# Optimization experiments

Measured on AMD Instinct MI355X. Metric: run time of the kernel, lower is better.

Reference implementation:

```python
import jax, jax.numpy as jnp
import numpy as np

EMBED_DIM = 768
NUM_HEADS = 12
HEAD_DIM = EMBED_DIM // NUM_HEADS
BSZ = 8
N = 1024


def setup_inputs() -> dict:
    key = jax.random.key(0)
    ks = jax.random.split(key, 11)
    s = 1.0 / np.sqrt(EMBED_DIM)
    return {
        "query": jax.random.normal(ks[0], (BSZ, N, EMBED_DIM), dtype=jnp.float32),
        "attn_bias": jax.random.normal(ks[1], (BSZ, NUM_HEADS, N, N), dtype=jnp.float32),
        "Wq": jax.random.normal(ks[2], (EMBED_DIM, EMBED_DIM), dtype=jnp.float32) * s,
        "bq": jax.random.normal(ks[3], (EMBED_DIM,), dtype=jnp.float32) * 0.01,
        "Wk": jax.random.normal(ks[4], (EMBED_DIM, EMBED_DIM), dtype=jnp.float32) * s,
        "bk": jax.random.normal(ks[5], (EMBED_DIM,), dtype=jnp.float32) * 0.01,
        "Wv": jax.random.normal(ks[6], (EMBED_DIM, EMBED_DIM), dtype=jnp.float32) * s,
        "bv": jax.random.normal(ks[7], (EMBED_DIM,), dtype=jnp.float32) * 0.01,
        "Wo": jax.random.normal(ks[8], (EMBED_DIM, EMBED_DIM), dtype=jnp.float32) * s,
        "bo": jnp.zeros((EMBED_DIM,), dtype=jnp.float32),
    }


def reference(query, attn_bias, Wq, bq, Wk, bk, Wv, bv, Wo, bo):
    # query: (b, n, e); weights stored torch-style (out, in): y = x @ W.T + b
    b, n, e = query.shape
    h, d = NUM_HEADS, HEAD_DIM
    scaling = d ** -0.5

    q = (query @ Wq.T + bq) * scaling          # (b, n, e)
    k = query @ Wk.T + bk
    v = query @ Wv.T + bv

    # split heads -> (b, h, n, d)
    q = q.reshape(b, n, h, d).transpose(0, 2, 1, 3)
    k = k.reshape(b, n, h, d).transpose(0, 2, 1, 3)
    v = v.reshape(b, n, h, d).transpose(0, 2, 1, 3)

    scores = jnp.einsum("bhqd,bhkd->bhqk", q, k) + attn_bias  # (b, h, n, n)
    probs = jax.nn.softmax(scores, axis=-1)
    attn = jnp.einsum("bhqk,bhkd->bhqd", probs, v)             # (b, h, n, d)

    attn = attn.transpose(0, 2, 1, 3).reshape(b, n, e)
    return attn @ Wo.T + bo
```

## Files before the change

kernel.cpp:

```cpp
#include <hip/hip_runtime.h>
#include <math.h>


namespace {

constexpr int kB = 8, kN = 1024, kE = 768, kH = 12, kD = 64;
constexpr int kM = kB * kN;
constexpr int kNX = kM * kE;
constexpr int kNW = kE * kE;
constexpr int kTot = kNX + 4 * kNW;

typedef short bf16x8 __attribute__((ext_vector_type(8)));
typedef float f32x4 __attribute__((ext_vector_type(4)));

__device__ __forceinline__ ushort f2bf(float x) {
  uint u = __float_as_uint(x);
  u += 0x7fffu + ((u >> 16) & 1u);
  return (ushort)(u >> 16);
}
__device__ __forceinline__ float bf2f(ushort h) {
  return __uint_as_float(((uint)h) << 16);
}

__global__ __launch_bounds__(256)
void split_convert(const float* __restrict__ X, const float* __restrict__ Wq,
                   const float* __restrict__ Wk, const float* __restrict__ Wv,
                   const float* __restrict__ Wo, ushort* __restrict__ Xh,
                   ushort* __restrict__ Xl, ushort* __restrict__ Wh,
                   ushort* __restrict__ Wl) {
  const int gid = blockIdx.x * 256 + threadIdx.x;
  const int i4 = gid * 4;
  if (i4 >= kTot) return;
  const float* s;
  ushort *dh, *dl;
  if (i4 < kNX) {
    s = X + i4;
    dh = Xh + i4;
    dl = Xl + i4;
  } else {
    const int j = i4 - kNX;
    const int w = j / kNW;
    const int o = j - w * kNW;
    s = (w == 0) ? Wq + o : (w == 1) ? Wk + o : (w == 2) ? Wv + o : Wo + o;
    dh = Wh + j;
    dl = Wl + j;
  }
  const float4 v = *(const float4*)s;
  ushort4 h, l;
  h.x = f2bf(v.x);
  h.y = f2bf(v.y);
  h.z = f2bf(v.z);
  h.w = f2bf(v.w);
  l.x = f2bf(v.x - bf2f(h.x));
  l.y = f2bf(v.y - bf2f(h.y));
  l.z = f2bf(v.z - bf2f(h.z));
  l.w = f2bf(v.w - bf2f(h.w));
  *(ushort4*)dh = h;
  *(ushort4*)dl = l;
}

__global__ __launch_bounds__(256)
void split_attn(const float* __restrict__ A, ushort* __restrict__ Ah,
                ushort* __restrict__ Al) {
  const int i4 = (blockIdx.x * 256 + threadIdx.x) * 4;
  if (i4 >= kNX) return;
  const float4 v = *(const float4*)(A + i4);
  ushort4 h, l;
  h.x = f2bf(v.x);
  h.y = f2bf(v.y);
  h.z = f2bf(v.z);
  h.w = f2bf(v.w);
  l.x = f2bf(v.x - bf2f(h.x));
  l.y = f2bf(v.y - bf2f(h.y));
  l.z = f2bf(v.z - bf2f(h.z));
  l.w = f2bf(v.w - bf2f(h.w));
  *(ushort4*)(Ah + i4) = h;
  *(ushort4*)(Al + i4) = l;
}

struct Frag44 {
  f32x4 a[4][4];
};

template <typename EPI>
__device__ __forceinline__ void gemm_core(const ushort* __restrict__ Ahg,
                                          const ushort* __restrict__ Alg,
                                          const ushort* __restrict__ Bhg,
                                          const ushort* __restrict__ Blg,
                                          int m0, int o0, EPI epi) {
  __shared__ ushort Ah[128][40], Al[128][40], Bh[128][40], Bl[128][40];
  const int tid = threadIdx.x;
  const int wid = tid >> 6, lane = tid & 63;
  const int wm = wid >> 1, wn = wid & 1;
  const int g = lane >> 4, lr = lane & 15;

  f32x4 acc[4][4];
#pragma unroll
  for (int i = 0; i < 4; ++i)
#pragma unroll
    for (int j = 0; j < 4; ++j) acc[i][j] = (f32x4)0.f;

  for (int k0 = 0; k0 < kE; k0 += 32) {
#pragma unroll
    for (int p = 0; p < 4; ++p) {
      const int f = tid + p * 256;
      const int m = f >> 3, kq = f & 7;
      const int ga = (m0 + m) * kE + k0 + kq * 4;
      const int gb = (o0 + m) * kE + k0 + kq * 4;
      *(uint2*)&Ah[m][kq * 4] = *(const uint2*)&Ahg[ga];
      *(uint2*)&Al[m][kq * 4] = *(const uint2*)&Alg[ga];
      *(uint2*)&Bh[m][kq * 4] = *(const uint2*)&Bhg[gb];
      *(uint2*)&Bl[m][kq * 4] = *(const uint2*)&Blg[gb];
    }
    __syncthreads();

    bf16x8 ah[4], al[4];
#pragma unroll
    for (int mi = 0; mi < 4; ++mi) {
      const int ar = wm * 64 + mi * 16 + lr;
      ah[mi] = *reinterpret_cast<const bf16x8*>(&Ah[ar][g * 8]);
      al[mi] = *reinterpret_cast<const bf16x8*>(&Al[ar][g * 8]);
    }
#pragma unroll
    for (int nj = 0; nj < 4; ++nj) {
      const int br = wn * 64 + nj * 16 + lr;
      const bf16x8 bh = *reinterpret_cast<const bf16x8*>(&Bh[br][g * 8]);
      const bf16x8 bl = *reinterpret_cast<const bf16x8*>(&Bl[br][g * 8]);
#pragma unroll
      for (int mi = 0; mi < 4; ++mi) {
        acc[mi][nj] = __builtin_amdgcn_mfma_f32_16x16x32_bf16(ah[mi], bh,
                                                              acc[mi][nj], 0, 0, 0);
        acc[mi][nj] = __builtin_amdgcn_mfma_f32_16x16x32_bf16(ah[mi], bl,
                                                              acc[mi][nj], 0, 0, 0);
        acc[mi][nj] = __builtin_amdgcn_mfma_f32_16x16x32_bf16(al[mi], bh,
                                                              acc[mi][nj], 0, 0, 0);
      }
    }
    __syncthreads();
  }

#pragma unroll
  for (int nj = 0; nj < 4; ++nj) {
    const int o = o0 + wn * 64 + nj * 16 + lr;
#pragma unroll
    for (int mi = 0; mi < 4; ++mi) {
      const int mbase = m0 + wm * 64 + mi * 16 + g * 4;
#pragma unroll
      for (int r = 0; r < 4; ++r) epi(mbase + r, o, acc[mi][nj][r]);
    }
  }
}

__global__ __launch_bounds__(256)
void qkv_gemm(const ushort* __restrict__ Xh, const ushort* __restrict__ Xl,
              const ushort* __restrict__ Wh, const ushort* __restrict__ Wl,
              const float* __restrict__ bq, const float* __restrict__ bk,
              const float* __restrict__ bv, float* __restrict__ Qo,
              float* __restrict__ Ko, float* __restrict__ Vo) {
  const int z = blockIdx.z;
  const ushort* WhZ = Wh + (size_t)z * kNW;
  const ushort* WlZ = Wl + (size_t)z * kNW;
  const float* bb = (z == 0) ? bq : (z == 1) ? bk : bv;
  float* Y = (z == 0) ? Qo : (z == 1) ? Ko : Vo;
  const float scale = (z == 0) ? 0.125f : 1.0f;

  gemm_core(Xh, Xl, WhZ, WlZ, blockIdx.x * 128, blockIdx.y * 128,
            [=](int m, int o, float v) {
              const int bi = m >> 10, n = m & 1023;
              const int h = o >> 6, d = o & 63;
              Y[(((size_t)bi * kH + h) * kN + n) * kD + d] = (v + bb[o]) * scale;
            });
}

__global__ __launch_bounds__(256)
void out_gemm(const ushort* __restrict__ Ahg, const ushort* __restrict__ Alg,
              const ushort* __restrict__ Wh, const ushort* __restrict__ Wl,
              const float* __restrict__ bo, float* __restrict__ Y) {
  gemm_core(Ahg, Alg, Wh, Wl, blockIdx.x * 128, blockIdx.y * 128,
            [=](int m, int o, float v) { Y[(size_t)m * kE + o] = v + bo[o]; });
}

__global__ __launch_bounds__(256)
void attn_kernel(const float* __restrict__ Q, const float* __restrict__ K,
                 const float* __restrict__ V, const float* __restrict__ bias,
                 float* __restrict__ Ao) {
  __shared__ float Qs[64][64];
  __shared__ float Ks[64][64];
  __shared__ float Vs[64][64];
  __shared__ float St[64][65];
  __shared__ float red[4][64];
  __shared__ float mrow[64], lrow[64], srow[64];

  const int n0 = blockIdx.x * 64;
  const int h = blockIdx.y, b = blockIdx.z;
  const int tid = threadIdx.x;
  const int ty = tid >> 4, tx = tid & 15;
  const int i0 = ty * 4, j0 = tx * 4, d0 = tx * 4;
  const int irow = tid & 63, qtr = tid >> 6;

  const size_t headoff = ((size_t)(b * kH + h)) * kN * kD;
  const float* __restrict__ Qh = Q + headoff;
  const float* __restrict__ Kh = K + headoff;
  const float* __restrict__ Vh = V + headoff;
  const float* __restrict__ biash = bias + ((size_t)(b * kH + h)) * kN * kN;

#pragma unroll
  for (int p = 0; p < 4; ++p) {
    const int r = (tid >> 4) + p * 16;
    const int dq = (tid & 15) * 4;
    const float4 v4 = *(const float4*)&Qh[(size_t)(n0 + r) * kD + dq];
    Qs[dq + 0][r] = v4.x;
    Qs[dq + 1][r] = v4.y;
    Qs[dq + 2][r] = v4.z;
    Qs[dq + 3][r] = v4.w;
  }
  if (tid < 64) {
    mrow[tid] = -__builtin_inff();
    lrow[tid] = 0.f;
  }
  float O[4][4];
#pragma unroll
  for (int i = 0; i < 4; ++i)
#pragma unroll
    for (int j = 0; j < 4; ++j) O[i][j] = 0.f;
  __syncthreads();

  for (int t = 0; t < 16; ++t) {
    const int jg = t * 64;
#pragma unroll
    for (int p = 0; p < 4; ++p) {
      const int r = (tid >> 4) + p * 16;
      const int dq = (tid & 15) * 4;
      const float4 kv = *(const float4*)&Kh[(size_t)(jg + r) * kD + dq];
      Ks[dq + 0][r] = kv.x;
      Ks[dq + 1][r] = kv.y;
      Ks[dq + 2][r] = kv.z;
      Ks[dq + 3][r] = kv.w;
      *(float4*)&Vs[r][dq] = *(const float4*)&Vh[(size_t)(jg + r) * kD + dq];
    }
    __syncthreads();

    float s[4][4];
#pragma unroll
    for (int i = 0; i < 4; ++i)
#pragma unroll
      for (int j = 0; j < 4; ++j) s[i][j] = 0.f;
    for (int d = 0; d < 64; ++d) {
      float a[4], kb[4];
      *(float4*)&a[0] = *(const float4*)&Qs[d][i0];
      *(float4*)&kb[0] = *(const float4*)&Ks[d][j0];
#pragma unroll
      for (int i = 0; i < 4; ++i)
#pragma unroll
        for (int j = 0; j < 4; ++j) s[i][j] = fmaf(a[i], kb[j], s[i][j]);
    }
#pragma unroll
    for (int i = 0; i < 4; ++i) {
      const float4 bv4 =
          *(const float4*)&biash[(size_t)(n0 + i0 + i) * kN + jg + j0];
      St[j0 + 0][i0 + i] = s[i][0] + bv4.x;
      St[j0 + 1][i0 + i] = s[i][1] + bv4.y;
      St[j0 + 2][i0 + i] = s[i][2] + bv4.z;
      St[j0 + 3][i0 + i] = s[i][3] + bv4.w;
    }
    __syncthreads();

    float pm = -__builtin_inff();
#pragma unroll
    for (int j = 0; j < 16; ++j) pm = fmaxf(pm, St[qtr * 16 + j][irow]);
    red[qtr][irow] = pm;
    __syncthreads();
    if (tid < 64) {
      const float tm = fmaxf(fmaxf(red[0][tid], red[1][tid]),
                             fmaxf(red[2][tid], red[3][tid]));
      const float mo = mrow[tid];
      const float mn = fmaxf(mo, tm);
      mrow[tid] = mn;
      srow[tid] = __expf(mo - mn);
    }
    __syncthreads();

    const float mi = mrow[irow];
    float ps = 0.f;
#pragma unroll
    for (int j = 0; j < 16; ++j) {
      const float e = __expf(St[qtr * 16 + j][irow] - mi);
      St[qtr * 16 + j][irow] = e;
      ps += e;
    }
    red[qtr][irow] = ps;
    __syncthreads();
    if (tid < 64)
      lrow[tid] = lrow[tid] * srow[tid] +
                  (red[0][tid] + red[1][tid] + red[2][tid] + red[3][tid]);

    float sf[4];
#pragma unroll
    for (int i = 0; i < 4; ++i) sf[i] = srow[i0 + i];
#pragma unroll
    for (int i = 0; i < 4; ++i)
#pragma unroll
      for (int j = 0; j < 4; ++j) O[i][j] *= sf[i];
#pragma unroll 8
    for (int j = 0; j < 64; ++j) {
      const float4 vv = *(const float4*)&Vs[j][d0];
      const float p0 = St[j][i0 + 0];
      const float p1 = St[j][i0 + 1];
      const float p2 = St[j][i0 + 2];
      const float p3 = St[j][i0 + 3];
      O[0][0] = fmaf(p0, vv.x, O[0][0]);
      O[0][1] = fmaf(p0, vv.y, O[0][1]);
      O[0][2] = fmaf(p0, vv.z, O[0][2]);
      O[0][3] = fmaf(p0, vv.w, O[0][3]);
      O[1][0] = fmaf(p1, vv.x, O[1][0]);
      O[1][1] = fmaf(p1, vv.y, O[1][1]);
      O[1][2] = fmaf(p1, vv.z, O[1][2]);
      O[1][3] = fmaf(p1, vv.w, O[1][3]);
      O[2][0] = fmaf(p2, vv.x, O[2][0]);
      O[2][1] = fmaf(p2, vv.y, O[2][1]);
      O[2][2] = fmaf(p2, vv.z, O[2][2]);
      O[2][3] = fmaf(p2, vv.w, O[2][3]);
      O[3][0] = fmaf(p3, vv.x, O[3][0]);
      O[3][1] = fmaf(p3, vv.y, O[3][1]);
      O[3][2] = fmaf(p3, vv.z, O[3][2]);
      O[3][3] = fmaf(p3, vv.w, O[3][3]);
    }
    __syncthreads();
  }

#pragma unroll
  for (int i = 0; i < 4; ++i) {
    const float inv = 1.0f / lrow[i0 + i];
    float4 r;
    r.x = O[i][0] * inv;
    r.y = O[i][1] * inv;
    r.z = O[i][2] * inv;
    r.w = O[i][3] * inv;
    *(float4*)&Ao[((size_t)b * kN + n0 + i0 + i) * kE + h * kD + d0] = r;
  }
}

}

extern "C" void kernel_launch(void* const* d_in, const int* in_sizes, int n_in,
                              void* d_out, int out_size, void* d_ws,
                              size_t ws_size, hipStream_t stream) {
  (void)in_sizes;
  (void)n_in;
  (void)out_size;
  (void)ws_size;
  const float* x = (const float*)d_in[0];
  const float* bias = (const float*)d_in[1];
  const float* Wq = (const float*)d_in[2];
  const float* bq = (const float*)d_in[3];
  const float* Wk = (const float*)d_in[4];
  const float* bk = (const float*)d_in[5];
  const float* Wv = (const float*)d_in[6];
  const float* bv = (const float*)d_in[7];
  const float* Wo = (const float*)d_in[8];
  const float* bo = (const float*)d_in[9];
  float* out = (float*)d_out;

  const size_t per = (size_t)kB * kH * kN * kD;
  float* q = (float*)d_ws;
  float* k = q + per;
  float* v = k + per;
  float* attn = v + per;
  ushort* Xh = (ushort*)(attn + per);
  ushort* Xl = Xh + kNX;
  ushort* Whs = Xl + kNX;
  ushort* Wls = Whs + 4 * (size_t)kNW;
  ushort* AttnH = Wls + 4 * (size_t)kNW;
  ushort* AttnL = AttnH + kNX;

  split_convert<<<kTot / 1024, 256, 0, stream>>>(x, Wq, Wk, Wv, Wo, Xh, Xl,
                                                 Whs, Wls);

  dim3 g1(kM / 128, kE / 128, 3);
  qkv_gemm<<<g1, 256, 0, stream>>>(Xh, Xl, Whs, Wls, bq, bk, bv, q, k, v);

  dim3 g2(kN / 64, kH, kB);
  attn_kernel<<<g2, 256, 0, stream>>>(q, k, v, bias, attn);

  split_attn<<<kNX / 1024, 256, 0, stream>>>(attn, AttnH, AttnL);

  dim3 g3(kM / 128, kE / 128);
  out_gemm<<<g3, 256, 0, stream>>>(AttnH, AttnL, Whs + 3 * (size_t)kNW,
                                   Wls + 3 * (size_t)kNW, bo, out);
}
```

Baseline: 1.086 ms.

## Rewrite attention with split-bf16 MFMA and fuse bf16 splitting into epilogues

Replaces the scalar FP32 attention kernel with a flash-style kernel that computes QK^T and PV using bf16 MFMA with hi/lo splitting (three products per step) to keep near-FP32 accuracy. The QKV GEMM epilogue now writes split bf16 Q, K and transposed V directly, and the attention kernel writes the split output, which removes the separate split_attn pass and the FP32 intermediate buffers. Blocks are mapped so that heads group by XCD. Softmax reductions use wave shuffles and per-wave LDS in place of block barriers, but K/V are read straight from global memory without LDS reuse and the epilogue stores are scalar and strided.

```diff
diff --git a/kernel.cpp b/kernel.cpp
--- a/kernel.cpp
+++ b/kernel.cpp
@@ -59,29 +59,6 @@
   *(ushort4*)dl = l;
 }
 
-__global__ __launch_bounds__(256)
-void split_attn(const float* __restrict__ A, ushort* __restrict__ Ah,
-                ushort* __restrict__ Al) {
-  const int i4 = (blockIdx.x * 256 + threadIdx.x) * 4;
-  if (i4 >= kNX) return;
-  const float4 v = *(const float4*)(A + i4);
-  ushort4 h, l;
-  h.x = f2bf(v.x);
-  h.y = f2bf(v.y);
-  h.z = f2bf(v.z);
-  h.w = f2bf(v.w);
-  l.x = f2bf(v.x - bf2f(h.x));
-  l.y = f2bf(v.y - bf2f(h.y));
-  l.z = f2bf(v.z - bf2f(h.z));
-  l.w = f2bf(v.w - bf2f(h.w));
-  *(ushort4*)(Ah + i4) = h;
-  *(ushort4*)(Al + i4) = l;
-}
-
-struct Frag44 {
-  f32x4 a[4][4];
-};
-
 template <typename EPI>
 __device__ __forceinline__ void gemm_core(const ushort* __restrict__ Ahg,
                                           const ushort* __restrict__ Alg,
@@ -155,21 +132,205 @@
 void qkv_gemm(const ushort* __restrict__ Xh, const ushort* __restrict__ Xl,
               const ushort* __restrict__ Wh, const ushort* __restrict__ Wl,
               const float* __restrict__ bq, const float* __restrict__ bk,
-              const float* __restrict__ bv, float* __restrict__ Qo,
-              float* __restrict__ Ko, float* __restrict__ Vo) {
+              const float* __restrict__ bv, ushort* __restrict__ Qh,
+              ushort* __restrict__ Ql, ushort* __restrict__ Kh,
+              ushort* __restrict__ Kl, ushort* __restrict__ Vth,
+              ushort* __restrict__ Vtl) {
   const int z = blockIdx.z;
   const ushort* WhZ = Wh + (size_t)z * kNW;
   const ushort* WlZ = Wl + (size_t)z * kNW;
   const float* bb = (z == 0) ? bq : (z == 1) ? bk : bv;
-  float* Y = (z == 0) ? Qo : (z == 1) ? Ko : Vo;
-  const float scale = (z == 0) ? 0.125f : 1.0f;
 
   gemm_core(Xh, Xl, WhZ, WlZ, blockIdx.x * 128, blockIdx.y * 128,
             [=](int m, int o, float v) {
               const int bi = m >> 10, n = m & 1023;
               const int h = o >> 6, d = o & 63;
-              Y[(((size_t)bi * kH + h) * kN + n) * kD + d] = (v + bb[o]) * scale;
+              const int head = bi * kH + h;
+              float val = v + bb[o];
+              if (z == 0) val *= 0.125f;
+              const ushort hi = f2bf(val);
+              const ushort lo = f2bf(val - bf2f(hi));
+              if (z == 2) {
+                const size_t idx = ((size_t)head * kD + d) * kN + n;
+                Vth[idx] = hi;
+                Vtl[idx] = lo;
+              } else {
+                const size_t idx = ((size_t)head * kN + n) * kD + d;
+                if (z == 0) {
+                  Qh[idx] = hi;
+                  Ql[idx] = lo;
+                } else {
+                  Kh[idx] = hi;
+                  Kl[idx] = lo;
+                }
+              }
             });
+}
+
+__global__ __launch_bounds__(256, 2)
+void attn_mfma(const ushort* __restrict__ Qhg, const ushort* __restrict__ Qlg,
+               const ushort* __restrict__ Khg, const ushort* __restrict__ Klg,
+               const ushort* __restrict__ Vth, const ushort* __restrict__ Vtl,
+               const float* __restrict__ bias, ushort* __restrict__ AoH,
+               ushort* __restrict__ AoL) {
+  __shared__ uint Plds[4][16 * 68];
+
+  const int lb = blockIdx.x;
+  const int xcd = lb & 7;
+  const int idx = lb >> 3;
+  const int lh = idx >> 4;
+  const int qb = idx & 15;
+  const int head = lh * 8 + xcd;
+  const int n0 = qb * 64;
+
+  const int tid = threadIdx.x;
+  const int w = tid >> 6, lane = tid & 63;
+  const int g = lane >> 4, c = lane & 15;
+
+  const size_t qkoff = (size_t)head * kN * kD;
+  const float* __restrict__ biash = bias + (size_t)head * kN * kN;
+  uint* __restrict__ Pw = &Plds[w][0];
+
+  bf16x8 qah[2], qal[2];
+#pragma unroll
+  for (int ks = 0; ks < 2; ++ks) {
+    const size_t qi = qkoff + (size_t)(n0 + w * 16 + c) * kD + ks * 32 + g * 8;
+    qah[ks] = *reinterpret_cast<const bf16x8*>(&Qhg[qi]);
+    qal[ks] = *reinterpret_cast<const bf16x8*>(&Qlg[qi]);
+  }
+
+  f32x4 o[4];
+#pragma unroll
+  for (int fd = 0; fd < 4; ++fd) o[fd] = (f32x4)0.f;
+  float m_old[4] = {-__builtin_inff(), -__builtin_inff(), -__builtin_inff(),
+                    -__builtin_inff()};
+  float lsum[4] = {0.f, 0.f, 0.f, 0.f};
+
+  for (int t = 0; t < 16; ++t) {
+    const int kvb = t * 64;
+
+    float bld[4][4];
+#pragma unroll
+    for (int j = 0; j < 4; ++j)
+#pragma unroll
+      for (int r = 0; r < 4; ++r)
+        bld[j][r] = biash[(size_t)(n0 + w * 16 + g * 4 + r) * kN + kvb +
+                          j * 16 + c];
+
+    f32x4 s[4];
+#pragma unroll
+    for (int j = 0; j < 4; ++j) s[j] = (f32x4)0.f;
+#pragma unroll
+    for (int j = 0; j < 4; ++j) {
+#pragma unroll
+      for (int ks = 0; ks < 2; ++ks) {
+        const size_t ki =
+            qkoff + (size_t)(kvb + j * 16 + c) * kD + ks * 32 + g * 8;
+        const bf16x8 kbh = *reinterpret_cast<const bf16x8*>(&Khg[ki]);
+        const bf16x8 kbl = *reinterpret_cast<const bf16x8*>(&Klg[ki]);
+        s[j] = __builtin_amdgcn_mfma_f32_16x16x32_bf16(qah[ks], kbh, s[j], 0, 0, 0);
+        s[j] = __builtin_amdgcn_mfma_f32_16x16x32_bf16(qal[ks], kbh, s[j], 0, 0, 0);
+        s[j] = __builtin_amdgcn_mfma_f32_16x16x32_bf16(qah[ks], kbl, s[j], 0, 0, 0);
+      }
+    }
+#pragma unroll
+    for (int j = 0; j < 4; ++j)
+#pragma unroll
+      for (int r = 0; r < 4; ++r) s[j][r] += bld[j][r];
+
+    float mt[4];
+#pragma unroll
+    for (int r = 0; r < 4; ++r)
+      mt[r] = fmaxf(fmaxf(s[0][r], s[1][r]), fmaxf(s[2][r], s[3][r]));
+#pragma unroll
+    for (int mask = 1; mask < 16; mask <<= 1)
+#pragma unroll
+      for (int r = 0; r < 4; ++r)
+        mt[r] = fmaxf(mt[r], __shfl_xor(mt[r], mask, 16));
+    float sc[4];
+#pragma unroll
+    for (int r = 0; r < 4; ++r) {
+      const float mn = fmaxf(m_old[r], mt[r]);
+      sc[r] = __expf(m_old[r] - mn);
+      m_old[r] = mn;
+    }
+    float rt[4] = {0.f, 0.f, 0.f, 0.f};
+#pragma unroll
+    for (int j = 0; j < 4; ++j)
+#pragma unroll
+      for (int r = 0; r < 4; ++r) {
+        const float p = __expf(s[j][r] - m_old[r]);
+        s[j][r] = p;
+        rt[r] += p;
+      }
+#pragma unroll
+    for (int mask = 1; mask < 16; mask <<= 1)
+#pragma unroll
+      for (int r = 0; r < 4; ++r) rt[r] += __shfl_xor(rt[r], mask, 16);
+#pragma unroll
+    for (int r = 0; r < 4; ++r) lsum[r] = lsum[r] * sc[r] + rt[r];
+#pragma unroll
+    for (int fd = 0; fd < 4; ++fd)
+#pragma unroll
+      for (int r = 0; r < 4; ++r) o[fd][r] *= sc[r];
+
+#pragma unroll
+    for (int j = 0; j < 4; ++j)
+#pragma unroll
+      for (int r = 0; r < 4; ++r) {
+        const float p = s[j][r];
+        const ushort hi = f2bf(p);
+        const ushort lo = f2bf(p - bf2f(hi));
+        Pw[(g * 4 + r) * 68 + j * 16 + c] = (uint)hi | ((uint)lo << 16);
+      }
+
+    __threadfence_block();
+
+#pragma unroll
+    for (int ks = 0; ks < 2; ++ks) {
+      const uint4 r0 = *(const uint4*)&Pw[c * 68 + ks * 32 + g * 8];
+      const uint4 r1 = *(const uint4*)&Pw[c * 68 + ks * 32 + g * 8 + 4];
+      union {
+        uint u[4];
+        bf16x8 v;
+      } ph, pl;
+      ph.u[0] = (r0.x & 0xffffu) | (r0.y << 16);
+      pl.u[0] = (r0.x >> 16) | (r0.y & 0xffff0000u);
+      ph.u[1] = (r0.z & 0xffffu) | (r0.w << 16);
+      pl.u[1] = (r0.z >> 16) | (r0.w & 0xffff0000u);
+      ph.u[2] = (r1.x & 0xffffu) | (r1.y << 16);
+      pl.u[2] = (r1.x >> 16) | (r1.y & 0xffff0000u);
+      ph.u[3] = (r1.z & 0xffffu) | (r1.w << 16);
+      pl.u[3] = (r1.z >> 16) | (r1.w & 0xffff0000u);
+#pragma unroll
+      for (int fd = 0; fd < 4; ++fd) {
+        const size_t vi =
+            ((size_t)head * kD + fd * 16 + c) * kN + kvb + ks * 32 + g * 8;
+        const bf16x8 vbh = *reinterpret_cast<const bf16x8*>(&Vth[vi]);
+        const bf16x8 vbl = *reinterpret_cast<const bf16x8*>(&Vtl[vi]);
+        o[fd] = __builtin_amdgcn_mfma_f32_16x16x32_bf16(ph.v, vbh, o[fd], 0, 0, 0);
+        o[fd] = __builtin_amdgcn_mfma_f32_16x16x32_bf16(pl.v, vbh, o[fd], 0, 0, 0);
+        o[fd] = __builtin_amdgcn_mfma_f32_16x16x32_bf16(ph.v, vbl, o[fd], 0, 0, 0);
+      }
+    }
+  }
+
+  const int bb_ = head / kH, hh = head - bb_ * kH;
+  float inv[4];
+#pragma unroll
+  for (int r = 0; r < 4; ++r) inv[r] = 1.0f / lsum[r];
+#pragma unroll
+  for (int fd = 0; fd < 4; ++fd)
+#pragma unroll
+    for (int r = 0; r < 4; ++r) {
+      const float val = o[fd][r] * inv[r];
+      const ushort hi = f2bf(val);
+      const ushort lo = f2bf(val - bf2f(hi));
+      const size_t oi = ((size_t)bb_ * kN + n0 + w * 16 + g * 4 + r) * kE +
+                        hh * kD + fd * 16 + c;
+      AoH[oi] = hi;
+      AoL[oi] = lo;
+    }
 }
 
 __global__ __launch_bounds__(256)
@@ -178,166 +339,6 @@
               const float* __restrict__ bo, float* __restrict__ Y) {
   gemm_core(Ahg, Alg, Wh, Wl, blockIdx.x * 128, blockIdx.y * 128,
             [=](int m, int o, float v) { Y[(size_t)m * kE + o] = v + bo[o]; });
-}
-
-__global__ __launch_bounds__(256)
-void attn_kernel(const float* __restrict__ Q, const float* __restrict__ K,
-                 const float* __restrict__ V, const float* __restrict__ bias,
-                 float* __restrict__ Ao) {
-  __shared__ float Qs[64][64];
-  __shared__ float Ks[64][64];
-  __shared__ float Vs[64][64];
-  __shared__ float St[64][65];
-  __shared__ float red[4][64];
-  __shared__ float mrow[64], lrow[64], srow[64];
-
-  const int n0 = blockIdx.x * 64;
-  const int h = blockIdx.y, b = blockIdx.z;
-  const int tid = threadIdx.x;
-  const int ty = tid >> 4, tx = tid & 15;
-  const int i0 = ty * 4, j0 = tx * 4, d0 = tx * 4;
-  const int irow = tid & 63, qtr = tid >> 6;
-
-  const size_t headoff = ((size_t)(b * kH + h)) * kN * kD;
-  const float* __restrict__ Qh = Q + headoff;
-  const float* __restrict__ Kh = K + headoff;
-  const float* __restrict__ Vh = V + headoff;
-  const float* __restrict__ biash = bias + ((size_t)(b * kH + h)) * kN * kN;
-
-#pragma unroll
-  for (int p = 0; p < 4; ++p) {
-    const int r = (tid >> 4) + p * 16;
-    const int dq = (tid & 15) * 4;
-    const float4 v4 = *(const float4*)&Qh[(size_t)(n0 + r) * kD + dq];
-    Qs[dq + 0][r] = v4.x;
-    Qs[dq + 1][r] = v4.y;
-    Qs[dq + 2][r] = v4.z;
-    Qs[dq + 3][r] = v4.w;
-  }
-  if (tid < 64) {
-    mrow[tid] = -__builtin_inff();
-    lrow[tid] = 0.f;
-  }
-  float O[4][4];
-#pragma unroll
-  for (int i = 0; i < 4; ++i)
-#pragma unroll
-    for (int j = 0; j < 4; ++j) O[i][j] = 0.f;
-  __syncthreads();
-
-  for (int t = 0; t < 16; ++t) {
-    const int jg = t * 64;
-#pragma unroll
-    for (int p = 0; p < 4; ++p) {
-      const int r = (tid >> 4) + p * 16;
-      const int dq = (tid & 15) * 4;
-      const float4 kv = *(const float4*)&Kh[(size_t)(jg + r) * kD + dq];
-      Ks[dq + 0][r] = kv.x;
-      Ks[dq + 1][r] = kv.y;
-      Ks[dq + 2][r] = kv.z;
-      Ks[dq + 3][r] = kv.w;
-      *(float4*)&Vs[r][dq] = *(const float4*)&Vh[(size_t)(jg + r) * kD + dq];
-    }
-    __syncthreads();
-
-    float s[4][4];
-#pragma unroll
-    for (int i = 0; i < 4; ++i)
-#pragma unroll
-      for (int j = 0; j < 4; ++j) s[i][j] = 0.f;
-    for (int d = 0; d < 64; ++d) {
-      float a[4], kb[4];
-      *(float4*)&a[0] = *(const float4*)&Qs[d][i0];
-      *(float4*)&kb[0] = *(const float4*)&Ks[d][j0];
-#pragma unroll
-      for (int i = 0; i < 4; ++i)
-#pragma unroll
-        for (int j = 0; j < 4; ++j) s[i][j] = fmaf(a[i], kb[j], s[i][j]);
-    }
-#pragma unroll
-    for (int i = 0; i < 4; ++i) {
-      const float4 bv4 =
-          *(const float4*)&biash[(size_t)(n0 + i0 + i) * kN + jg + j0];
-      St[j0 + 0][i0 + i] = s[i][0] + bv4.x;
-      St[j0 + 1][i0 + i] = s[i][1] + bv4.y;
-      St[j0 + 2][i0 + i] = s[i][2] + bv4.z;
-      St[j0 + 3][i0 + i] = s[i][3] + bv4.w;
-    }
-    __syncthreads();
-
-    float pm = -__builtin_inff();
-#pragma unroll
-    for (int j = 0; j < 16; ++j) pm = fmaxf(pm, St[qtr * 16 + j][irow]);
-    red[qtr][irow] = pm;
-    __syncthreads();
-    if (tid < 64) {
-      const float tm = fmaxf(fmaxf(red[0][tid], red[1][tid]),
-                             fmaxf(red[2][tid], red[3][tid]));
-      const float mo = mrow[tid];
-      const float mn = fmaxf(mo, tm);
-      mrow[tid] = mn;
-      srow[tid] = __expf(mo - mn);
-    }
-    __syncthreads();
-
-    const float mi = mrow[irow];
-    float ps = 0.f;
-#pragma unroll
-    for (int j = 0; j < 16; ++j) {
-      const float e = __expf(St[qtr * 16 + j][irow] - mi);
-      St[qtr * 16 + j][irow] = e;
-      ps += e;
-    }
-    red[qtr][irow] = ps;
-    __syncthreads();
-    if (tid < 64)
-      lrow[tid] = lrow[tid] * srow[tid] +
-                  (red[0][tid] + red[1][tid] + red[2][tid] + red[3][tid]);
-
-    float sf[4];
-#pragma unroll
-    for (int i = 0; i < 4; ++i) sf[i] = srow[i0 + i];
-#pragma unroll
-    for (int i = 0; i < 4; ++i)
-#pragma unroll
-      for (int j = 0; j < 4; ++j) O[i][j] *= sf[i];
-#pragma unroll 8
-    for (int j = 0; j < 64; ++j) {
-      const float4 vv = *(const float4*)&Vs[j][d0];
-      const float p0 = St[j][i0 + 0];
-      const float p1 = St[j][i0 + 1];
-      const float p2 = St[j][i0 + 2];
-      const float p3 = St[j][i0 + 3];
-      O[0][0] = fmaf(p0, vv.x, O[0][0]);
-      O[0][1] = fmaf(p0, vv.y, O[0][1]);
-      O[0][2] = fmaf(p0, vv.z, O[0][2]);
-      O[0][3] = fmaf(p0, vv.w, O[0][3]);
-      O[1][0] = fmaf(p1, vv.x, O[1][0]);
-      O[1][1] = fmaf(p1, vv.y, O[1][1]);
-      O[1][2] = fmaf(p1, vv.z, O[1][2]);
-      O[1][3] = fmaf(p1, vv.w, O[1][3]);
-      O[2][0] = fmaf(p2, vv.x, O[2][0]);
-      O[2][1] = fmaf(p2, vv.y, O[2][1]);
-      O[2][2] = fmaf(p2, vv.z, O[2][2]);
-      O[2][3] = fmaf(p2, vv.w, O[2][3]);
-      O[3][0] = fmaf(p3, vv.x, O[3][0]);
-      O[3][1] = fmaf(p3, vv.y, O[3][1]);
-      O[3][2] = fmaf(p3, vv.z, O[3][2]);
-      O[3][3] = fmaf(p3, vv.w, O[3][3]);
-    }
-    __syncthreads();
-  }
-
-#pragma unroll
-  for (int i = 0; i < 4; ++i) {
-    const float inv = 1.0f / lrow[i0 + i];
-    float4 r;
-    r.x = O[i][0] * inv;
-    r.y = O[i][1] * inv;
-    r.z = O[i][2] * inv;
-    r.w = O[i][3] * inv;
-    *(float4*)&Ao[((size_t)b * kN + n0 + i0 + i) * kE + h * kD + d0] = r;
-  }
 }
 
 }
@@ -361,28 +362,40 @@
   const float* bo = (const float*)d_in[9];
   float* out = (float*)d_out;
 
-  const size_t per = (size_t)kB * kH * kN * kD;
-  float* q = (float*)d_ws;
-  float* k = q + per;
-  float* v = k + per;
-  float* attn = v + per;
-  ushort* Xh = (ushort*)(attn + per);
-  ushort* Xl = Xh + kNX;
-  ushort* Whs = Xl + kNX;
-  ushort* Wls = Whs + 4 * (size_t)kNW;
-  ushort* AttnH = Wls + 4 * (size_t)kNW;
-  ushort* AttnL = AttnH + kNX;
+  ushort* p = (ushort*)d_ws;
+  ushort* QhA = p;
+  p += kNX;
+  ushort* QlA = p;
+  p += kNX;
+  ushort* KhA = p;
+  p += kNX;
+  ushort* KlA = p;
+  p += kNX;
+  ushort* VthA = p;
+  p += kNX;
+  ushort* VtlA = p;
+  p += kNX;
+  ushort* Xh = p;
+  p += kNX;
+  ushort* Xl = p;
+  p += kNX;
+  ushort* Whs = p;
+  p += 4 * (size_t)kNW;
+  ushort* Wls = p;
+  p += 4 * (size_t)kNW;
+  ushort* AttnH = p;
+  p += kNX;
+  ushort* AttnL = p;
 
   split_convert<<<kTot / 1024, 256, 0, stream>>>(x, Wq, Wk, Wv, Wo, Xh, Xl,
                                                  Whs, Wls);
 
   dim3 g1(kM / 128, kE / 128, 3);
-  qkv_gemm<<<g1, 256, 0, stream>>>(Xh, Xl, Whs, Wls, bq, bk, bv, q, k, v);
-
-  dim3 g2(kN / 64, kH, kB);
-  attn_kernel<<<g2, 256, 0, stream>>>(q, k, v, bias, attn);
-
-  split_attn<<<kNX / 1024, 256, 0, stream>>>(attn, AttnH, AttnL);
+  qkv_gemm<<<g1, 256, 0, stream>>>(Xh, Xl, Whs, Wls, bq, bk, bv, QhA, QlA,
+                                   KhA, KlA, VthA, VtlA);
+
+  attn_mfma<<<1536, 256, 0, stream>>>(QhA, QlA, KhA, KlA, VthA, VtlA, bias,
+                                      AttnH, AttnL);
 
   dim3 g3(kM / 128, kE / 128);
   out_gemm<<<g3, 256, 0, stream>>>(AttnH, AttnL, Whs + 3 * (size_t)kNW,
```

New measurement: 1.141 ms. 5.1% more time.
